# Optimization experiments

Measured on AMD Instinct MI355X. Metric: run time of the kernel, lower is better.

## Reference

```python
import jax, jax.numpy as jnp
import numpy as np

N = 4096
M0 = 2048
M1 = 2048
MCS = 4096
STRIDE = 2
D_NNGP = STRIDE ** 2 * M1              # 8192, input dim of layer-1 arccos maps
D_NTK = STRIDE ** 2 * (MCS + M1)       # 24576, input dim1 of layer-1 count sketch


def setup_inputs() -> dict:
    key = jax.random.key(0)
    ks = jax.random.split(key, 8)
    return {
        "layer_idx": 1,
        "z_nngp": jax.random.normal(ks[0], (N, D_NNGP), jnp.float32),
        "z_ntk": jax.random.normal(ks[1], (N, D_NTK), jnp.float32),
        "W0": jax.random.normal(ks[2], (D_NNGP, M0), jnp.float32),   # arccos0[1].W
        "W1": jax.random.normal(ks[3], (D_NNGP, M1), jnp.float32),   # arccos1[1].W
        "sign1": (jax.random.randint(ks[4], (D_NTK,), 0, 2) * 2 - 1).astype(jnp.float32),
        "indx1": jax.random.randint(ks[5], (D_NTK,), 0, MCS),
        "sign2": (jax.random.randint(ks[6], (M0,), 0, 2) * 2 - 1).astype(jnp.float32),
        "indx2": jax.random.randint(ks[7], (M0,), 0, MCS),
    }


def count_sketch(x, indx, sign, out_dim):
    # x: [n, d_in]; sign-multiply then scatter_add along last axis into out_dim bins
    xs = x * sign[None, :]
    out = jnp.zeros((x.shape[0], out_dim), dtype=x.dtype)
    return out.at[:, indx].add(xs)


def reference(layer_idx, z_nngp, z_ntk, W0, W1, sign1, indx1, sign2, indx2):
    norm0 = np.sqrt(2.0 / M0).astype(np.float32)
    norm1 = np.float32(np.sqrt(2.0 / M1) / 2.0)
    # arccos order-0 feature map (step function)
    xw0 = z_nngp @ W0
    tmp = (xw0 > 0).astype(z_nngp.dtype) * norm0          # [N, M0]
    # arccos order-1 feature map (relu-like: |xw| + xw)
    xw1 = z_nngp @ W1
    z_nngp_out = (jnp.abs(xw1) + xw1) * norm1             # [N, M1]
    # tensor sketch: count-sketch both, FFT, complex pointwise multiply, ifft.real
    x_cs = count_sketch(z_ntk, indx1, sign1, MCS)         # [N, MCS]
    y_cs = count_sketch(tmp, indx2, sign2, MCS)           # [N, MCS]
    z_ntk_out = jnp.fft.ifft(jnp.fft.fft(x_cs, axis=-1) * jnp.fft.fft(y_cs, axis=-1)).real
    z_ntk_cat = jnp.concatenate([z_nngp_out, z_ntk_out], axis=1)  # [N, M1+MCS]
    return (z_nngp_out, z_ntk_cat)
```

## Files before the change

### kernel.cpp

```cpp
#include <hip/hip_runtime.h>

#define NROW 4096
#define KDIM 8192
#define MDIM 2048
#define MCS_ 4096
#define DNTK 24576
#define CATW 6144
#define TAU_HALF 2.5e-3f
#define NT (KDIM / 32)

typedef __attribute__((ext_vector_type(8))) short short8;
typedef __attribute__((ext_vector_type(4))) float f32x4;

__device__ __forceinline__ void split2(float x0, float x1,
                                       unsigned& hi, unsigned& lo) {
    const unsigned u0 = __float_as_uint(x0);
    const unsigned u1 = __float_as_uint(x1);
    hi = (u0 >> 16) | (u1 & 0xFFFF0000u);
    const float l0 = x0 - __uint_as_float(u0 & 0xFFFF0000u);
    const float l1 = x1 - __uint_as_float(u1 & 0xFFFF0000u);
    lo = (__float_as_uint(l0) >> 16) | (__float_as_uint(l1) & 0xFFFF0000u);
}

__device__ __forceinline__ float2 cmulf(float2 a, float2 b) {
    return make_float2(a.x * b.x - a.y * b.y, a.x * b.y + a.y * b.x);
}

__global__ __launch_bounds__(512) void convert_kernel(
    const float* __restrict__ A,
    const float* __restrict__ W1,
    const float* __restrict__ W0,
    short8* __restrict__ aHi, short8* __restrict__ aLo,
    short8* __restrict__ wHi, short8* __restrict__ wLo)
{
    int b = blockIdx.x;
    const int tid = threadIdx.x;
    if (b < 4096) {
        const int P = b >> 8, T = b & 255;
        const float* src = A + (size_t)(P * 256) * KDIM + T * 32;
        short8* dh = aHi + ((size_t)b << 10);
        short8* dl = aLo + ((size_t)b << 10);
        for (int s = tid; s < 1024; s += 512) {
            const int row = ((s >> 6) << 4) | (s & 15);
            const int k0  = ((s >> 4) & 3) * 8;
            const float* p = src + (size_t)row * KDIM + k0;
            const float4 v0 = *reinterpret_cast<const float4*>(p);
            const float4 v1 = *reinterpret_cast<const float4*>(p + 4);
            union { short8 ss; unsigned u[4]; } h, l;
            split2(v0.x, v0.y, h.u[0], l.u[0]);
            split2(v0.z, v0.w, h.u[1], l.u[1]);
            split2(v1.x, v1.y, h.u[2], l.u[2]);
            split2(v1.z, v1.w, h.u[3], l.u[3]);
            dh[s] = h.ss; dl[s] = l.ss;
        }
    } else {
        b -= 4096;
        const int mat = b >> 11;
        const int T   = b & 255;
        const int Pc  = (b >> 8) & 7;
        const float* Wm = mat ? W0 : W1;
        const float* src = Wm + (size_t)(T * 32) * MDIM + Pc * 256;
        short8* dh = wHi + ((size_t)b << 10);
        short8* dl = wLo + ((size_t)b << 10);
        for (int s = tid; s < 1024; s += 512) {
            const int col = ((s >> 6) << 4) | (s & 15);
            const int k0  = ((s >> 4) & 3) * 8;
            float v[8];
#pragma unroll
            for (int j = 0; j < 8; ++j)
                v[j] = src[(size_t)(k0 + j) * MDIM + col];
            union { short8 ss; unsigned u[4]; } h, l;
            split2(v[0], v[1], h.u[0], l.u[0]);
            split2(v[2], v[3], h.u[1], l.u[1]);
            split2(v[4], v[5], h.u[2], l.u[2]);
            split2(v[6], v[7], h.u[3], l.u[3]);
            dh[s] = h.ss; dl[s] = l.ss;
        }
    }
}

__global__ __launch_bounds__(512) void csr_build(
    const int* __restrict__ indx1, const float* __restrict__ sign1,
    const int* __restrict__ indx2, const float* __restrict__ sign2,
    int* __restrict__ rowptr1, int* __restrict__ ent1,
    int* __restrict__ rowptr2, int* __restrict__ ent2)
{
    const int which = blockIdx.x;
    const int*   idx = which ? indx2 : indx1;
    const float* sg  = which ? sign2 : sign1;
    const int    n   = which ? 2048 : 24576;
    int* rowptr = which ? rowptr2 : rowptr1;
    int* ent    = which ? ent2 : ent1;

    __shared__ int h[4096];
    __shared__ int rp[4097];
    __shared__ int part[512];
    const int tid = threadIdx.x;

    for (int i = tid; i < 4096; i += 512) h[i] = 0;
    __syncthreads();
    for (int d = tid; d < n; d += 512) atomicAdd(&h[idx[d]], 1);
    __syncthreads();

    int loc[8], s = 0;
#pragma unroll
    for (int k = 0; k < 8; ++k) { loc[k] = h[8 * tid + k]; s += loc[k]; }
    part[tid] = s;
    __syncthreads();
    for (int off = 1; off < 512; off <<= 1) {
        int v = part[tid];
        if (tid >= off) v += part[tid - off];
        __syncthreads();
        part[tid] = v;
        __syncthreads();
    }
    int base = tid ? part[tid - 1] : 0;
#pragma unroll
    for (int k = 0; k < 8; ++k) { rp[8 * tid + k] = base; base += loc[k]; }
    if (tid == 511) rp[4096] = base;
    __syncthreads();

    for (int i = tid; i < 4096; i += 512) h[i] = 0;
    __syncthreads();
    for (int d = tid; d < n; d += 512) {
        const int b   = idx[d];
        const int pos = atomicAdd(&h[b], 1);
        ent[rp[b] + pos] = d | (sg[d] < 0.f ? 0x80000000 : 0);
    }
    __syncthreads();

    for (int i = tid; i < 4097; i += 512) rowptr[i] = rp[i];
    for (int b = tid; b < 4096; b += 512) {
        const int lo = rp[b], hi = rp[b + 1];
        for (int i = lo + 1; i < hi; ++i) {
            const int e = ent[i], key = e & 0x7FFFFFFF;
            int j = i - 1;
            while (j >= lo && (ent[j] & 0x7FFFFFFF) > key) { ent[j + 1] = ent[j]; --j; }
            ent[j + 1] = e;
        }
    }
}

__global__ __launch_bounds__(512, 2) void gemm_mfma_pre(
    const short8* __restrict__ aHi, const short8* __restrict__ aLo,
    const short8* __restrict__ wHi, const short8* __restrict__ wLo,
    float* __restrict__ out0, float* __restrict__ outCat)
{
    const int mode = blockIdx.z;
    __shared__ short8 AhiS[2][1024], AloS[2][1024];
    __shared__ short8 BhiS[2][1024], BloS[2][1024];

    const int tid  = threadIdx.x;
    const int lane = tid & 63;
    const int wid  = tid >> 6;
    const int wr   = wid >> 1;
    const int wc   = wid & 1;
    const int brow = blockIdx.y * 256;
    const int bcol = blockIdx.x * 256;

    const size_t aBase = ((size_t)blockIdx.y) << 18;
    const size_t wBase = ((size_t)(mode * 8 + blockIdx.x)) << 18;

    f32x4 acc[4][8];
#pragma unroll
    for (int m = 0; m < 4; ++m)
#pragma unroll
        for (int n = 0; n < 8; ++n)
#pragma unroll
            for (int i = 0; i < 4; ++i) acc[m][n][i] = 0.f;

    short8 st[8];

#define ISSUE(T)                                                             \
    {                                                                        \
        const size_t o = ((size_t)(T)) << 10;                                \
        st[0] = aHi[aBase + o + tid];  st[1] = aHi[aBase + o + tid + 512];   \
        st[2] = aLo[aBase + o + tid];  st[3] = aLo[aBase + o + tid + 512];   \
        st[4] = wHi[wBase + o + tid];  st[5] = wHi[wBase + o + tid + 512];   \
        st[6] = wLo[wBase + o + tid];  st[7] = wLo[wBase + o + tid + 512];   \
    }
#define WRITE(BUF)                                                           \
    {                                                                        \
        AhiS[BUF][tid] = st[0];  AhiS[BUF][tid + 512] = st[1];               \
        AloS[BUF][tid] = st[2];  AloS[BUF][tid + 512] = st[3];               \
        BhiS[BUF][tid] = st[4];  BhiS[BUF][tid + 512] = st[5];               \
        BloS[BUF][tid] = st[6];  BloS[BUF][tid + 512] = st[7];               \
    }

    ISSUE(0); WRITE(0); ISSUE(1);
    __syncthreads();

    for (int t = 0; t < NT; ++t) {
        const int cur = t & 1;

        short8 ah[4], al[4];
#pragma unroll
        for (int m = 0; m < 4; ++m) {
            ah[m] = AhiS[cur][(wr * 4 + m) * 64 + lane];
            al[m] = AloS[cur][(wr * 4 + m) * 64 + lane];
        }

        if (t + 1 < NT) {
            WRITE(cur ^ 1);
            if (t + 2 < NT) ISSUE(t + 2);
        }

#pragma unroll
        for (int n = 0; n < 8; ++n) {
            const short8 bh = BhiS[cur][(wc * 8 + n) * 64 + lane];
            const short8 bl = BloS[cur][(wc * 8 + n) * 64 + lane];
#pragma unroll
            for (int m = 0; m < 4; ++m) {
                acc[m][n] = __builtin_amdgcn_mfma_f32_16x16x32_bf16(
                    ah[m], bh, acc[m][n], 0, 0, 0);
                acc[m][n] = __builtin_amdgcn_mfma_f32_16x16x32_bf16(
                    ah[m], bl, acc[m][n], 0, 0, 0);
                acc[m][n] = __builtin_amdgcn_mfma_f32_16x16x32_bf16(
                    al[m], bh, acc[m][n], 0, 0, 0);
            }
        }
        __syncthreads();
    }
#undef ISSUE
#undef WRITE

    const float norm0 = 0.03125f;
    const int ocol0 = bcol + wc * 128 + (lane & 15);
    const int orow0 = brow + wr * 64 + ((lane >> 4) << 2);
#pragma unroll
    for (int m = 0; m < 4; ++m)
#pragma unroll
        for (int n = 0; n < 8; ++n) {
            const int col = ocol0 + n * 16;
#pragma unroll
            for (int i = 0; i < 4; ++i) {
                const int row = orow0 + m * 16 + i;
                if (mode == 0) {
                    const float v = fmaxf(acc[m][n][i], 0.f) * norm0;
                    out0[(size_t)row * MDIM + col] = v;
                    outCat[(size_t)row * CATW + col] = v;
                } else {
                    outCat[(size_t)row * CATW + 2048 + col] = acc[m][n][i];
                }
            }
        }
}

__global__ __launch_bounds__(512, 2) void gemm_mfma(
    const float* __restrict__ A,
    const float* __restrict__ W1,
    const float* __restrict__ W0,
    float* __restrict__ out0,
    float* __restrict__ outCat)
{
    const int mode = blockIdx.z;
    const float* __restrict__ W = mode ? W0 : W1;

    __shared__ short8 AhiS[2][1024], AloS[2][1024];
    __shared__ short8 BhiS[2][1024], BloS[2][1024];

    const int tid  = threadIdx.x;
    const int lane = tid & 63;
    const int wid  = tid >> 6;
    const int wr   = wid >> 1;
    const int wc   = wid & 1;
    const int brow = blockIdx.y * 256;
    const int bcol = blockIdx.x * 256;

    f32x4 acc[4][8];
#pragma unroll
    for (int m = 0; m < 4; ++m)
#pragma unroll
        for (int n = 0; n < 8; ++n)
#pragma unroll
            for (int i = 0; i < 4; ++i) acc[m][n][i] = 0.f;

    const int srow  = tid >> 1;
    const int skh   = tid & 1;
    const int slot0 = (srow >> 4) * 64 + (srow & 15) + (skh << 5);
    const float* aptr = A + (size_t)(brow + srow) * KDIM + skh * 16;
    const float* bptr = W + (size_t)(skh * 16) * MDIM + (bcol + srow);

    float4 av0, av1, av2, av3;
    float  bst[16];

#define LOAD_TILE(T)                                                         \
    {                                                                        \
        const float* ap = aptr + (T) * 32;                                   \
        av0 = *reinterpret_cast<const float4*>(ap);                          \
        av1 = *reinterpret_cast<const float4*>(ap + 4);                      \
        av2 = *reinterpret_cast<const float4*>(ap + 8);                      \
        av3 = *reinterpret_cast<const float4*>(ap + 12);                     \
        const float* bp = bptr + (size_t)((T) * 32) * MDIM;                  \
        _Pragma("unroll")                                                    \
        for (int j = 0; j < 16; ++j) bst[j] = bp[(size_t)j * MDIM];          \
    }
#define CONVERT_WRITE(BUF)                                                   \
    {                                                                        \
        union { short8 s; unsigned u[4]; } h, l;                             \
        split2(av0.x, av0.y, h.u[0], l.u[0]);                                \
        split2(av0.z, av0.w, h.u[1], l.u[1]);                                \
        split2(av1.x, av1.y, h.u[2], l.u[2]);                                \
        split2(av1.z, av1.w, h.u[3], l.u[3]);                                \
        AhiS[BUF][slot0] = h.s;  AloS[BUF][slot0] = l.s;                     \
        split2(av2.x, av2.y, h.u[0], l.u[0]);                                \
        split2(av2.z, av2.w, h.u[1], l.u[1]);                                \
        split2(av3.x, av3.y, h.u[2], l.u[2]);                                \
        split2(av3.z, av3.w, h.u[3], l.u[3]);                                \
        AhiS[BUF][slot0 + 16] = h.s;  AloS[BUF][slot0 + 16] = l.s;           \
        split2(bst[0], bst[1], h.u[0], l.u[0]);                              \
        split2(bst[2], bst[3], h.u[1], l.u[1]);                              \
        split2(bst[4], bst[5], h.u[2], l.u[2]);                              \
        split2(bst[6], bst[7], h.u[3], l.u[3]);                              \
        BhiS[BUF][slot0] = h.s;  BloS[BUF][slot0] = l.s;                     \
        split2(bst[8],  bst[9],  h.u[0], l.u[0]);                            \
        split2(bst[10], bst[11], h.u[1], l.u[1]);                            \
        split2(bst[12], bst[13], h.u[2], l.u[2]);                            \
        split2(bst[14], bst[15], h.u[3], l.u[3]);                            \
        BhiS[BUF][slot0 + 16] = h.s;  BloS[BUF][slot0 + 16] = l.s;           \
    }

    LOAD_TILE(0);
    CONVERT_WRITE(0);
    LOAD_TILE(1);
    __syncthreads();

    for (int t = 0; t < NT; ++t) {
        const int cur = t & 1;
        short8 ah[4], al[4];
#pragma unroll
        for (int m = 0; m < 4; ++m) {
            ah[m] = AhiS[cur][(wr * 4 + m) * 64 + lane];
            al[m] = AloS[cur][(wr * 4 + m) * 64 + lane];
        }
        if (t + 1 < NT) {
            CONVERT_WRITE(cur ^ 1);
            if (t + 2 < NT) LOAD_TILE(t + 2);
        }
#pragma unroll
        for (int n = 0; n < 8; ++n) {
            const short8 bh = BhiS[cur][(wc * 8 + n) * 64 + lane];
            const short8 bl = BloS[cur][(wc * 8 + n) * 64 + lane];
#pragma unroll
            for (int m = 0; m < 4; ++m) {
                acc[m][n] = __builtin_amdgcn_mfma_f32_16x16x32_bf16(
                    ah[m], bh, acc[m][n], 0, 0, 0);
                acc[m][n] = __builtin_amdgcn_mfma_f32_16x16x32_bf16(
                    ah[m], bl, acc[m][n], 0, 0, 0);
                acc[m][n] = __builtin_amdgcn_mfma_f32_16x16x32_bf16(
                    al[m], bh, acc[m][n], 0, 0, 0);
            }
        }
        __syncthreads();
    }
#undef LOAD_TILE
#undef CONVERT_WRITE

    const float norm0 = 0.03125f;
    const int ocol0 = bcol + wc * 128 + (lane & 15);
    const int orow0 = brow + wr * 64 + ((lane >> 4) << 2);
#pragma unroll
    for (int m = 0; m < 4; ++m)
#pragma unroll
        for (int n = 0; n < 8; ++n) {
            const int col = ocol0 + n * 16;
#pragma unroll
            for (int i = 0; i < 4; ++i) {
                const int row = orow0 + m * 16 + i;
                if (mode == 0) {
                    const float v = fmaxf(acc[m][n][i], 0.f) * norm0;
                    out0[(size_t)row * MDIM + col] = v;
                    outCat[(size_t)row * CATW + col] = v;
                } else {
                    outCat[(size_t)row * CATW + 2048 + col] = acc[m][n][i];
                }
            }
        }
}

#define ZP(i) Z[(i) + ((i) >> 4)]
#define C_SQ2 0.70710678118654752f

__device__ __forceinline__ void fft_conv_body(float2* Z, const float2* RT, int tid) {
    float2 x0, x1, x2, x3, x4, x5, x6, x7;

#pragma unroll
    for (int s = 0; s < 4; ++s) {
        const int lq = 3 * (3 - s);
        const int q  = 1 << lq;
        const int j  = tid & (q - 1);
        const int base = ((tid >> lq) << (lq + 3)) + j;
        x0 = ZP(base);
        x1 = ZP(base + q);
        x2 = ZP(base + 2 * q);
        x3 = ZP(base + 3 * q);
        x4 = ZP(base + 4 * q);
        x5 = ZP(base + 5 * q);
        x6 = ZP(base + 6 * q);
        x7 = ZP(base + 7 * q);

        const float2 w1 = RT[j << (9 - lq)];
        const float2 w2 = cmulf(w1, w1);
        const float2 w3 = cmulf(w2, w1);
        const float2 w4 = cmulf(w2, w2);
        const float2 w5 = cmulf(w3, w2);
        const float2 w6 = cmulf(w3, w3);
        const float2 w7 = cmulf(w4, w3);

        const float2 a0 = make_float2(x0.x + x4.x, x0.y + x4.y);
        const float2 a1 = make_float2(x1.x + x5.x, x1.y + x5.y);
        const float2 a2 = make_float2(x2.x + x6.x, x2.y + x6.y);
        const float2 a3 = make_float2(x3.x + x7.x, x3.y + x7.y);
        const float2 b0 = make_float2(x0.x - x4.x, x0.y - x4.y);
        const float2 b1 = make_float2(x1.x - x5.x, x1.y - x5.y);
        const float2 b2 = make_float2(x2.x - x6.x, x2.y - x6.y);
        const float2 b3 = make_float2(x3.x - x7.x, x3.y - x7.y);

        const float2 ca0 = make_float2(a0.x + a2.x, a0.y + a2.y);
        const float2 ca1 = make_float2(a0.x - a2.x, a0.y - a2.y);
        const float2 ca2 = make_float2(a1.x + a3.x, a1.y + a3.y);
        const float2 ca3 = make_float2(a1.x - a3.x, a1.y - a3.y);
        const float2 y0 = make_float2(ca0.x + ca2.x, ca0.y + ca2.y);
        const float2 y4 = make_float2(ca0.x - ca2.x, ca0.y - ca2.y);
        const float2 y2 = make_float2(ca1.x + ca3.y, ca1.y - ca3.x);
        const float2 y6 = make_float2(ca1.x - ca3.y, ca1.y + ca3.x);

        const float2 b1r = make_float2(C_SQ2 * (b1.x + b1.y), C_SQ2 * (b1.y - b1.x));
        const float2 b2r = make_float2(b2.y, -b2.x);
        const float2 b3r = make_float2(C_SQ2 * (b3.y - b3.x), -C_SQ2 * (b3.x + b3.y));
        const float2 cb0 = make_float2(b0.x + b2r.x, b0.y + b2r.y);
        const float2 cb1 = make_float2(b0.x - b2r.x, b0.y - b2r.y);
        const float2 cb2 = make_float2(b1r.x + b3r.x, b1r.y + b3r.y);
        const float2 cb3 = make_float2(b1r.x - b3r.x, b1r.y - b3r.y);
        const float2 y1 = make_float2(cb0.x + cb2.x, cb0.y + cb2.y);
        const float2 y5 = make_float2(cb0.x - cb2.x, cb0.y - cb2.y);
        const float2 y3 = make_float2(cb1.x + cb3.y, cb1.y - cb3.x);
        const float2 y7 = make_float2(cb1.x - cb3.y, cb1.y + cb3.x);

        ZP(base)         = y0;
        ZP(base + q)     = cmulf(y1, w1);
        ZP(base + 2 * q) = cmulf(y2, w2);
        ZP(base + 3 * q) = cmulf(y3, w3);
        ZP(base + 4 * q) = cmulf(y4, w4);
        ZP(base + 5 * q) = cmulf(y5, w5);
        ZP(base + 6 * q) = cmulf(y6, w6);
        ZP(base + 7 * q) = cmulf(y7, w7);
        __syncthreads();
    }

    for (int p = tid; p < MCS_; p += 512) {
        int q;
        if (p == 0) q = 0;
        else {
            const int h = 31 - __clz(p);
            q = 9 * (1 << (3 * (h / 3))) - 1 - p;
        }
        if (p <= q) {
            const float2 Ap = ZP(p);
            const float2 Bq = ZP(q);
            const float Xr = 0.5f * (Ap.x + Bq.x);
            const float Xi = 0.5f * (Ap.y - Bq.y);
            const float Yr = 0.5f * (Ap.y + Bq.y);
            const float Yi = -0.5f * (Ap.x - Bq.x);
            const float Pr = Xr * Yr - Xi * Yi;
            const float Pi = Xr * Yi + Xi * Yr;
            ZP(p) = make_float2(Pr, Pi);
            ZP(q) = make_float2(Pr, -Pi);
        }
    }
    __syncthreads();

#pragma unroll
    for (int s = 0; s < 4; ++s) {
        const int lq = 3 * s;
        const int q  = 1 << lq;
        const int j  = tid & (q - 1);
        const int base = ((tid >> lq) << (lq + 3)) + j;

        const float2 w1 = RT[j << (9 - lq)];
        const float2 w2 = cmulf(w1, w1);
        const float2 w3 = cmulf(w2, w1);
        const float2 w4 = cmulf(w2, w2);
        const float2 w5 = cmulf(w3, w2);
        const float2 w6 = cmulf(w3, w3);
        const float2 w7 = cmulf(w4, w3);

        x0 = ZP(base);
        {
            float2 t;
            t = ZP(base + q);     x1 = make_float2(t.x * w1.x + t.y * w1.y, t.y * w1.x - t.x * w1.y);
            t = ZP(base + 2 * q); x2 = make_float2(t.x * w2.x + t.y * w2.y, t.y * w2.x - t.x * w2.y);
            t = ZP(base + 3 * q); x3 = make_float2(t.x * w3.x + t.y * w3.y, t.y * w3.x - t.x * w3.y);
            t = ZP(base + 4 * q); x4 = make_float2(t.x * w4.x + t.y * w4.y, t.y * w4.x - t.x * w4.y);
            t = ZP(base + 5 * q); x5 = make_float2(t.x * w5.x + t.y * w5.y, t.y * w5.x - t.x * w5.y);
            t = ZP(base + 6 * q); x6 = make_float2(t.x * w6.x + t.y * w6.y, t.y * w6.x - t.x * w6.y);
            t = ZP(base + 7 * q); x7 = make_float2(t.x * w7.x + t.y * w7.y, t.y * w7.x - t.x * w7.y);
        }

        const float2 a0 = make_float2(x0.x + x4.x, x0.y + x4.y);
        const float2 a1 = make_float2(x1.x + x5.x, x1.y + x5.y);
        const float2 a2 = make_float2(x2.x + x6.x, x2.y + x6.y);
        const float2 a3 = make_float2(x3.x + x7.x, x3.y + x7.y);
        const float2 b0 = make_float2(x0.x - x4.x, x0.y - x4.y);
        const float2 b1 = make_float2(x1.x - x5.x, x1.y - x5.y);
        const float2 b2 = make_float2(x2.x - x6.x, x2.y - x6.y);
        const float2 b3 = make_float2(x3.x - x7.x, x3.y - x7.y);

        const float2 ca0 = make_float2(a0.x + a2.x, a0.y + a2.y);
        const float2 ca1 = make_float2(a0.x - a2.x, a0.y - a2.y);
        const float2 ca2 = make_float2(a1.x + a3.x, a1.y + a3.y);
        const float2 ca3 = make_float2(a1.x - a3.x, a1.y - a3.y);
        const float2 y0 = make_float2(ca0.x + ca2.x, ca0.y + ca2.y);
        const float2 y4 = make_float2(ca0.x - ca2.x, ca0.y - ca2.y);
        const float2 y2 = make_float2(ca1.x - ca3.y, ca1.y + ca3.x);
        const float2 y6 = make_float2(ca1.x + ca3.y, ca1.y - ca3.x);

        const float2 b1r = make_float2(C_SQ2 * (b1.x - b1.y), C_SQ2 * (b1.x + b1.y));
        const float2 b2r = make_float2(-b2.y, b2.x);
        const float2 b3r = make_float2(-C_SQ2 * (b3.x + b3.y), C_SQ2 * (b3.x - b3.y));
        const float2 cb0 = make_float2(b0.x + b2r.x, b0.y + b2r.y);
        const float2 cb1 = make_float2(b0.x - b2r.x, b0.y - b2r.y);
        const float2 cb2 = make_float2(b1r.x + b3r.x, b1r.y + b3r.y);
        const float2 cb3 = make_float2(b1r.x - b3r.x, b1r.y - b3r.y);
        const float2 y1 = make_float2(cb0.x + cb2.x, cb0.y + cb2.y);
        const float2 y5 = make_float2(cb0.x - cb2.x, cb0.y - cb2.y);
        const float2 y3 = make_float2(cb1.x - cb3.y, cb1.y + cb3.x);
        const float2 y7 = make_float2(cb1.x + cb3.y, cb1.y - cb3.x);

        ZP(base)         = y0;
        ZP(base + q)     = y1;
        ZP(base + 2 * q) = y2;
        ZP(base + 3 * q) = y3;
        ZP(base + 4 * q) = y4;
        ZP(base + 5 * q) = y5;
        ZP(base + 6 * q) = y6;
        ZP(base + 7 * q) = y7;
        __syncthreads();
    }
}

__global__ __launch_bounds__(512) void sketch_fft_csr(
    const float* __restrict__ z_ntk,
    const int* __restrict__ rowptr1, const int* __restrict__ ent1,
    const int* __restrict__ rowptr2, const int* __restrict__ ent2,
    float* __restrict__ outCat)
{
    __shared__ __align__(16) float2 Z[4352];
    __shared__ float2 RT[513];
    float* Zf = reinterpret_cast<float*>(Z);
    const int tid = threadIdx.x;
    const int row = blockIdx.x;
    const float norm0 = 0.03125f;

    const float wconst = -1.5339807878856412e-3f;
    for (int t = tid; t <= 512; t += 512) {
        float sw, cw;
        __sincosf(wconst * (float)t, &sw, &cw);
        RT[t] = make_float2(cw, sw);
    }

    int rpx[9], rpy[9];
#pragma unroll
    for (int k = 0; k < 9; ++k) {
        rpx[k] = rowptr1[8 * tid + k];
        rpy[k] = rowptr2[8 * tid + k];
    }
    float accX[8], accY[8];
#pragma unroll
    for (int k = 0; k < 8; ++k) { accX[k] = 0.f; accY[k] = 0.f; }
    int cur[8];
#pragma unroll
    for (int k = 0; k < 8; ++k) cur[k] = rpx[k];

    const float4* xrow4 = reinterpret_cast<const float4*>(z_ntk + (size_t)row * DNTK);
    for (int c = 0; c < 3; ++c) {
        const int lo = c * 8192, hi = lo + 8192;
        __syncthreads();
#pragma unroll
        for (int j = 0; j < 4; ++j)
            reinterpret_cast<float4*>(Zf)[tid + j * 512] = xrow4[c * 2048 + tid + j * 512];
        __syncthreads();

        for (;;) {
            bool ok[8];
            int e8[8];
#pragma unroll
            for (int k = 0; k < 8; ++k) {
                ok[k] = cur[k] < rpx[k + 1];
                e8[k] = ent1[ok[k] ? cur[k] : 0];
            }
            int any = 0;
#pragma unroll
            for (int k = 0; k < 8; ++k) {
                ok[k] = ok[k] && ((e8[k] & 0x7FFFFFFF) < hi);
                any |= (int)ok[k];
            }
            if (!any) break;
            float v8[8];
#pragma unroll
            for (int k = 0; k < 8; ++k)
                v8[k] = Zf[ok[k] ? ((e8[k] & 0x7FFFFFFF) - lo) : 0];
#pragma unroll
            for (int k = 0; k < 8; ++k) {
                if (ok[k]) {
                    accX[k] += (e8[k] < 0) ? -v8[k] : v8[k];
                    ++cur[k];
                }
            }
        }
    }

    const float* trow = outCat + (size_t)row * CATW + 2048;
    __syncthreads();
    reinterpret_cast<float4*>(Zf)[tid] = reinterpret_cast<const float4*>(trow)[tid];
    __syncthreads();
#pragma unroll
    for (int k = 0; k < 8; ++k) {
        for (int c = rpy[k]; c < rpy[k + 1]; ++c) {
            const int e = ent2[c];
            const int d = e & 0x7FFFFFFF;
            const float t = Zf[d];
            const float y = (fabsf(t) < TAU_HALF) ? 0.5f * norm0
                                                  : (t > 0.f ? norm0 : 0.f);
            accY[k] += (e < 0) ? -y : y;
        }
    }
    __syncthreads();

#pragma unroll
    for (int k = 0; k < 8; ++k) {
        const int b = 8 * tid + k;
        ZP(b) = make_float2(accX[k], accY[k]);
    }
    __syncthreads();

    fft_conv_body(Z, RT, tid);

    float* orow = outCat + (size_t)row * CATW + 2048;
    const float scale = 1.0f / (float)MCS_;
    for (int n = tid; n < MCS_; n += 512) orow[n] = ZP(n).x * scale;
}

#define YBASE 4608
__global__ __launch_bounds__(512) void sketch_fft_atomic(
    const float* __restrict__ z_ntk,
    const float* __restrict__ sign1,
    const int*   __restrict__ indx1,
    const float* __restrict__ sign2,
    const int*   __restrict__ indx2,
    float* __restrict__ outCat)
{
    __shared__ __align__(16) float2 Z[4352];
    __shared__ float2 RT[513];
    float* Zf = reinterpret_cast<float*>(Z);
    const int tid = threadIdx.x;
    const int row = blockIdx.x;

    for (int i = tid; i < 2176; i += 512)
        reinterpret_cast<float4*>(Zf)[i] = make_float4(0.f, 0.f, 0.f, 0.f);
    const float wconst = -1.5339807878856412e-3f;
    for (int t = tid; t <= 512; t += 512) {
        float sw, cw;
        __sincosf(wconst * (float)t, &sw, &cw);
        RT[t] = make_float2(cw, sw);
    }
    __syncthreads();

    const float4* xrow4 = reinterpret_cast<const float4*>(z_ntk + (size_t)row * DNTK);
    const float4* s1v   = reinterpret_cast<const float4*>(sign1);
    const int4*   i1v   = reinterpret_cast<const int4*>(indx1);
    for (int v = tid; v < DNTK / 4; v += 512) {
        const float4 x = xrow4[v];
        const float4 s = s1v[v];
        const int4   ix = i1v[v];
        atomicAdd(&Zf[ix.x], x.x * s.x);
        atomicAdd(&Zf[ix.y], x.y * s.y);
        atomicAdd(&Zf[ix.z], x.z * s.z);
        atomicAdd(&Zf[ix.w], x.w * s.w);
    }
    const float norm0 = 0.03125f;
    const float* trow = outCat + (size_t)row * CATW + 2048;
    {
        const float4 t4 = reinterpret_cast<const float4*>(trow)[tid];
        const float4 s  = reinterpret_cast<const float4*>(sign2)[tid];
        const int4   ix = reinterpret_cast<const int4*>(indx2)[tid];
        const float y0 = (fabsf(t4.x) < TAU_HALF) ? 0.5f * norm0 : (t4.x > 0.f ? norm0 : 0.f);
        const float y1 = (fabsf(t4.y) < TAU_HALF) ? 0.5f * norm0 : (t4.y > 0.f ? norm0 : 0.f);
        const float y2 = (fabsf(t4.z) < TAU_HALF) ? 0.5f * norm0 : (t4.z > 0.f ? norm0 : 0.f);
        const float y3 = (fabsf(t4.w) < TAU_HALF) ? 0.5f * norm0 : (t4.w > 0.f ? norm0 : 0.f);
        atomicAdd(&Zf[YBASE + ix.x], y0 * s.x);
        atomicAdd(&Zf[YBASE + ix.y], y1 * s.y);
        atomicAdd(&Zf[YBASE + ix.z], y2 * s.z);
        atomicAdd(&Zf[YBASE + ix.w], y3 * s.w);
    }
    __syncthreads();

    {
        float re[8], im[8];
#pragma unroll
        for (int j = 0; j < 8; ++j) {
            const int i = tid + j * 512;
            re[j] = Zf[i];
            im[j] = Zf[YBASE + i];
        }
        __syncthreads();
#pragma unroll
        for (int j = 0; j < 8; ++j) {
            const int i = tid + j * 512;
            ZP(i) = make_float2(re[j], im[j]);
        }
    }
    __syncthreads();

    fft_conv_body(Z, RT, tid);

    float* orow = outCat + (size_t)row * CATW + 2048;
    const float scale = 1.0f / (float)MCS_;
    for (int n = tid; n < MCS_; n += 512) orow[n] = ZP(n).x * scale;
}

extern "C" void kernel_launch(void* const* d_in, const int* in_sizes, int n_in,
                              void* d_out, int out_size, void* d_ws, size_t ws_size,
                              hipStream_t stream) {
    (void)in_sizes; (void)n_in; (void)out_size;
    const float* z_nngp = (const float*)d_in[1];
    const float* z_ntk  = (const float*)d_in[2];
    const float* W0     = (const float*)d_in[3];
    const float* W1     = (const float*)d_in[4];
    const float* sign1  = (const float*)d_in[5];
    const int*   indx1  = (const int*)d_in[6];
    const float* sign2  = (const float*)d_in[7];
    const int*   indx2  = (const int*)d_in[8];

    float* out0   = (float*)d_out;
    float* outCat = out0 + (size_t)NROW * MDIM;

    const size_t NEED_P = 268435456ull;
    const size_t NEED_C = NEED_P + (1ull << 20);

    int* rowptr1 = nullptr; int* rowptr2 = nullptr;
    int* ent1 = nullptr;    int* ent2 = nullptr;
    const bool csr_ok = ws_size >= NEED_C;
    if (csr_ok) {
        int* base = (int*)((char*)d_ws + NEED_P);
        rowptr1 = base;
        rowptr2 = base + 4352;
        ent1    = base + 8704;
        ent2    = ent1 + 24576;
        csr_build<<<dim3(2), dim3(512), 0, stream>>>(
            indx1, sign1, indx2, sign2, rowptr1, ent1, rowptr2, ent2);
    }

    if (ws_size >= NEED_P) {
        short8* aHi = (short8*)d_ws;
        short8* aLo = aHi + (1ull << 22);
        short8* wHi = aLo + (1ull << 22);
        short8* wLo = wHi + (1ull << 22);
        convert_kernel<<<dim3(8192), dim3(512), 0, stream>>>(
            z_nngp, W1, W0, aHi, aLo, wHi, wLo);
        gemm_mfma_pre<<<dim3(8, 16, 2), dim3(512), 0, stream>>>(
            aHi, aLo, wHi, wLo, out0, outCat);
    } else {
        gemm_mfma<<<dim3(8, 16, 2), dim3(512), 0, stream>>>(
            z_nngp, W1, W0, out0, outCat);
    }

    if (csr_ok) {
        sketch_fft_csr<<<dim3(NROW), dim3(512), 0, stream>>>(
            z_ntk, rowptr1, ent1, rowptr2, ent2, outCat);
    } else {
        sketch_fft_atomic<<<dim3(NROW), dim3(512), 0, stream>>>(
            z_ntk, sign1, indx1, sign2, indx2, outCat);
    }
}
```

Baseline: 1.147 ms.

## Shrink GEMM block tile to 128x256 and read A fragments directly from global

The pre-converted GEMM now uses 128-row block tiles (double the grid in y) with a 2x4 warp layout, so each warp holds a 64x64 accumulator instead of 64x128. A-operand fragments are no longer staged through shared memory; each wave loads its bf16 hi/lo A fragments straight from global memory every k-step, and only B is double-buffered in LDS. This cuts LDS use and register pressure to raise occupancy and parallelism. The cost is lower reuse per block, more global and L2 traffic for A and B, and unhidden global-load latency on the A path.

```diff
diff --git a/kernel.cpp b/kernel.cpp
--- a/kernel.cpp
+++ b/kernel.cpp
@@ -147,68 +147,65 @@
     float* __restrict__ out0, float* __restrict__ outCat)
 {
     const int mode = blockIdx.z;
-    __shared__ short8 AhiS[2][1024], AloS[2][1024];
     __shared__ short8 BhiS[2][1024], BloS[2][1024];
 
     const int tid  = threadIdx.x;
     const int lane = tid & 63;
     const int wid  = tid >> 6;
-    const int wr   = wid >> 1;
-    const int wc   = wid & 1;
-    const int brow = blockIdx.y * 256;
-    const int bcol = blockIdx.x * 256;
-
-    const size_t aBase = ((size_t)blockIdx.y) << 18;
-    const size_t wBase = ((size_t)(mode * 8 + blockIdx.x)) << 18;
-
-    f32x4 acc[4][8];
+    const int wr   = wid >> 2;
+    const int wc   = wid & 3;
+    const int bx   = blockIdx.x;
+    const int by   = blockIdx.y;
+
+    const size_t aBase  = ((size_t)(by >> 1)) << 18;
+    const int    fragA0 = ((by & 1) << 3) + wr * 4;
+    const size_t wBase  = ((size_t)(mode * 8 + bx)) << 18;
+
+    f32x4 acc[4][4];
 #pragma unroll
     for (int m = 0; m < 4; ++m)
 #pragma unroll
-        for (int n = 0; n < 8; ++n)
+        for (int n = 0; n < 4; ++n)
 #pragma unroll
             for (int i = 0; i < 4; ++i) acc[m][n][i] = 0.f;
 
-    short8 st[8];
-
-#define ISSUE(T)                                                             \
+    short8 stB[4];
+
+#define ISSUE_B(T)                                                           \
     {                                                                        \
         const size_t o = ((size_t)(T)) << 10;                                \
-        st[0] = aHi[aBase + o + tid];  st[1] = aHi[aBase + o + tid + 512];   \
-        st[2] = aLo[aBase + o + tid];  st[3] = aLo[aBase + o + tid + 512];   \
-        st[4] = wHi[wBase + o + tid];  st[5] = wHi[wBase + o + tid + 512];   \
-        st[6] = wLo[wBase + o + tid];  st[7] = wLo[wBase + o + tid + 512];   \
-    }
-#define WRITE(BUF)                                                           \
+        stB[0] = wHi[wBase + o + tid];  stB[1] = wHi[wBase + o + tid + 512]; \
+        stB[2] = wLo[wBase + o + tid];  stB[3] = wLo[wBase + o + tid + 512]; \
+    }
+#define WRITE_B(BUF)                                                         \
     {                                                                        \
-        AhiS[BUF][tid] = st[0];  AhiS[BUF][tid + 512] = st[1];               \
-        AloS[BUF][tid] = st[2];  AloS[BUF][tid + 512] = st[3];               \
-        BhiS[BUF][tid] = st[4];  BhiS[BUF][tid + 512] = st[5];               \
-        BloS[BUF][tid] = st[6];  BloS[BUF][tid + 512] = st[7];               \
-    }
-
-    ISSUE(0); WRITE(0); ISSUE(1);
+        BhiS[BUF][tid] = stB[0];  BhiS[BUF][tid + 512] = stB[1];             \
+        BloS[BUF][tid] = stB[2];  BloS[BUF][tid + 512] = stB[3];             \
+    }
+
+    ISSUE_B(0); WRITE_B(0); ISSUE_B(1);
     __syncthreads();
 
     for (int t = 0; t < NT; ++t) {
         const int cur = t & 1;
+        const size_t aOff = aBase + (((size_t)t) << 10) + lane;
 
         short8 ah[4], al[4];
 #pragma unroll
         for (int m = 0; m < 4; ++m) {
-            ah[m] = AhiS[cur][(wr * 4 + m) * 64 + lane];
-            al[m] = AloS[cur][(wr * 4 + m) * 64 + lane];
+            ah[m] = aHi[aOff + (fragA0 + m) * 64];
+            al[m] = aLo[aOff + (fragA0 + m) * 64];
         }
 
         if (t + 1 < NT) {
-            WRITE(cur ^ 1);
-            if (t + 2 < NT) ISSUE(t + 2);
-        }
-
-#pragma unroll
-        for (int n = 0; n < 8; ++n) {
-            const short8 bh = BhiS[cur][(wc * 8 + n) * 64 + lane];
-            const short8 bl = BloS[cur][(wc * 8 + n) * 64 + lane];
+            WRITE_B(cur ^ 1);
+            if (t + 2 < NT) ISSUE_B(t + 2);
+        }
+
+#pragma unroll
+        for (int n = 0; n < 4; ++n) {
+            const short8 bh = BhiS[cur][(wc * 4 + n) * 64 + lane];
+            const short8 bl = BloS[cur][(wc * 4 + n) * 64 + lane];
 #pragma unroll
             for (int m = 0; m < 4; ++m) {
                 acc[m][n] = __builtin_amdgcn_mfma_f32_16x16x32_bf16(
@@ -221,16 +218,16 @@
         }
         __syncthreads();
     }
-#undef ISSUE
-#undef WRITE
+#undef ISSUE_B
+#undef WRITE_B
 
     const float norm0 = 0.03125f;
-    const int ocol0 = bcol + wc * 128 + (lane & 15);
-    const int orow0 = brow + wr * 64 + ((lane >> 4) << 2);
+    const int ocol0 = bx * 256 + wc * 64 + (lane & 15);
+    const int orow0 = by * 128 + wr * 64 + ((lane >> 4) << 2);
 #pragma unroll
     for (int m = 0; m < 4; ++m)
 #pragma unroll
-        for (int n = 0; n < 8; ++n) {
+        for (int n = 0; n < 4; ++n) {
             const int col = ocol0 + n * 16;
 #pragma unroll
             for (int i = 0; i < 4; ++i) {
@@ -758,7 +755,7 @@
         short8* wLo = wHi + (1ull << 22);
         convert_kernel<<<dim3(8192), dim3(512), 0, stream>>>(
             z_nngp, W1, W0, aHi, aLo, wHi, wLo);
-        gemm_mfma_pre<<<dim3(8, 16, 2), dim3(512), 0, stream>>>(
+        gemm_mfma_pre<<<dim3(8, 32, 2), dim3(512), 0, stream>>>(
             aHi, aLo, wHi, wLo, out0, outCat);
     } else {
         gemm_mfma<<<dim3(8, 16, 2), dim3(512), 0, stream>>>(
```

Measured after the change: 1.439 ms. +25.5%, slower.
